# Kernel optimization log

Measured on AMD Instinct MI355X. Metric: run time of the kernel, lower is better.

## Reference

```python
import jax, jax.numpy as jnp
import numpy as np

H = 256  # hidden size

def setup_inputs() -> dict:
    key = jax.random.key(0)
    k1, k2, k3 = jax.random.split(key, 3)
    B, T, D = 64, 2048, 256
    x = jax.random.normal(k1, (B, T, D), dtype=jnp.float32)
    Wx = jax.random.normal(k2, (D, 4 * H), dtype=jnp.float32) * (1.0 / np.sqrt(D))
    Wh = jax.random.normal(k3, (H, 4 * H), dtype=jnp.float32) * (1.0 / np.sqrt(H))
    bx = jnp.zeros((4 * H,), dtype=jnp.float32)
    bh = jnp.zeros((4 * H,), dtype=jnp.float32)
    return {"x": x, "Wx": Wx, "Wh": Wh, "bx": bx, "bh": bh}

def reference(x, Wx, Wh, bx, bh):
    B, T, D = x.shape
    # Precompute input projections for all timesteps: [T, B, 4H]
    xg = jnp.einsum('btd,dg->tbg', x, Wx) + bx

    def step(carry, xg_t):
        h_prev, c_prev = carry
        gates = xg_t + h_prev @ Wh + bh          # [B, 4H]
        f, i, o, chat = jnp.split(gates, 4, axis=-1)
        f_t = jax.nn.sigmoid(f)
        i_t = jax.nn.sigmoid(i)
        o_t = jax.nn.sigmoid(o)
        c_t = f_t * c_prev + i_t * jnp.tanh(chat)
        h_t = o_t * jnp.tanh(c_t)
        return (h_t, c_t), h_t

    h0 = jnp.zeros((B, H), dtype=x.dtype)
    c0 = jnp.zeros((B, H), dtype=x.dtype)
    (h_T, c_T), hs = jax.lax.scan(step, (h0, c0), xg)  # hs: [T, B, H]
    outputs = jnp.transpose(hs, (1, 0, 2))  # batch_first: [B, T, H]
    return outputs, (h_T, c_T)
```

## Files before the change

kernel.cpp:

```cpp
#include <hip/hip_runtime.h>
#include <stdint.h>

#define H 256
#define BB 64
#define TT 2048
#define G4 1024
#define LDX 264

typedef __attribute__((ext_vector_type(8))) short short8;
typedef __attribute__((ext_vector_type(4))) float float4_;
typedef unsigned long long ull;
typedef unsigned short ushort_t;
typedef unsigned int uint_t;

static __device__ __forceinline__ float bfhi2f(ushort_t u) {
    union { unsigned int i; float f; } v; v.i = ((unsigned int)u) << 16; return v.f;
}
static __device__ __forceinline__ ushort_t f2bf(float x) {
    union { float f; unsigned int i; } v; v.f = x;
    unsigned int u = v.i;
    return (ushort_t)((u + 0x7FFFu + ((u >> 16) & 1u)) >> 16);
}
static __device__ __forceinline__ void split2(float x, ushort_t& hi, ushort_t& lo) {
    hi = f2bf(x);
    lo = f2bf(x - bfhi2f(hi));
}
static __device__ __forceinline__ float sigm(float x) { return 1.0f / (1.0f + __expf(-x)); }
static __device__ __forceinline__ float tanh_(float x) { return 2.0f / (1.0f + __expf(-2.0f * x)) - 1.0f; }

__global__ __launch_bounds__(256) void split_w(const float* __restrict__ Wx,
                                               const float* __restrict__ Wh,
                                               ushort_t* __restrict__ planes) {
    const int g = blockIdx.x & 1023;
    const int mat = blockIdx.x >> 10;
    const int k = threadIdx.x;
    const float* src = mat ? Wh : Wx;
    float v = src[(size_t)k * G4 + g];
    ushort_t hi, lo; split2(v, hi, lo);
    ushort_t* ph = planes + (size_t)mat * 2 * G4 * 256;
    ph[g * 256 + k] = hi;
    ph[(size_t)G4 * 256 + g * 256 + k] = lo;
}

__global__ __launch_bounds__(256, 1) void lstm_scan(
        const float* __restrict__ x,
        const float* __restrict__ bx,
        const float* __restrict__ bh,
        const ushort_t* __restrict__ WxTh, const ushort_t* __restrict__ WxTl,
        const ushort_t* __restrict__ WhTh, const ushort_t* __restrict__ WhTl,
        float* __restrict__ out0,
        float* __restrict__ outh,
        float* __restrict__ outc,
        uint_t* __restrict__ hbuf) {
    __shared__ ushort_t xah[16 * LDX], xal[16 * LDX];
    __shared__ ushort_t hsh[16 * LDX], hsl[16 * LDX];
    __shared__ float gatesL[1024];
    __shared__ float cst[256];
    __shared__ float bL[64];

    const int tid = threadIdx.x;
    const int grp = blockIdx.x & 3;
    const int s = blockIdx.x >> 2;
    const int lane = tid & 63, wave = tid >> 6;
    const int lm = lane & 15, lq = lane >> 4;
    const int pb = tid >> 4, pj = tid & 15;

    if (tid < 64) {
        int g = ((tid >> 4) << 8) + (s << 4) + (tid & 15);
        bL[tid] = bx[g] + bh[g];
    }
    cst[tid] = 0.0f;

    const size_t wrow = ((size_t)((wave << 8) + (s << 4) + lm)) * 256;
    short8 fxh[8], fxl[8], fhh[8], fhl[8];
#pragma unroll
    for (int kc = 0; kc < 8; ++kc) {
        fxh[kc] = *(const short8*)(WxTh + wrow + kc * 32 + lq * 8);
        fxl[kc] = *(const short8*)(WxTl + wrow + kc * 32 + lq * 8);
        fhh[kc] = *(const short8*)(WhTh + wrow + kc * 32 + lq * 8);
        fhl[kc] = *(const short8*)(WhTl + wrow + kc * 32 + lq * 8);
    }

    const float* xp0 = x + ((size_t)(grp * 16 + pb)) * TT * 256 + pj * 16;
    float* o0 = out0 + ((size_t)(grp * 16 + pb)) * TT * H + (s << 4) + pj;

    float4_ xv[4];
#pragma unroll
    for (int q = 0; q < 4; ++q) xv[q] = *(const float4_*)(xp0 + q * 4);

    const int rb = pb * LDX + pj * 16;

    for (int t = 0; t < TT; ++t) {
#pragma unroll
        for (int q = 0; q < 4; ++q) {
            union { ushort_t u[4]; ull q8; } ph_, pl_;
#pragma unroll
            for (int e = 0; e < 4; ++e) {
                ushort_t hi, lo; split2(xv[q][e], hi, lo);
                ph_.u[e] = hi; pl_.u[e] = lo;
            }
            *(ull*)(xah + rb + q * 4) = ph_.q8;
            *(ull*)(xal + rb + q * 4) = pl_.q8;
        }
        __syncthreads();

        const uint_t* hp = hbuf + ((((t & 1) << 2) + grp) << 12) + (pb << 8) + (pj << 4);
        uint_t w[16];
        if (t > 0) {
#pragma unroll
            for (int e = 0; e < 16; ++e)
                w[e] = __hip_atomic_load(hp + e, __ATOMIC_RELAXED, __HIP_MEMORY_SCOPE_AGENT);
        }

        float4_ acc = {};
#pragma unroll
        for (int kc = 0; kc < 8; ++kc) {
            short8 ah = *(const short8*)(xah + lm * LDX + kc * 32 + lq * 8);
            short8 al = *(const short8*)(xal + lm * LDX + kc * 32 + lq * 8);
            acc = __builtin_amdgcn_mfma_f32_16x16x32_bf16(ah, fxh[kc], acc, 0, 0, 0);
            acc = __builtin_amdgcn_mfma_f32_16x16x32_bf16(ah, fxl[kc], acc, 0, 0, 0);
            acc = __builtin_amdgcn_mfma_f32_16x16x32_bf16(al, fxh[kc], acc, 0, 0, 0);
        }

        if (t + 1 < TT) {
            const float* xp = xp0 + (size_t)(t + 1) * 256;
#pragma unroll
            for (int q = 0; q < 4; ++q) xv[q] = *(const float4_*)(xp + q * 4);
        }

        if (t > 0) {
            const uint_t texp = (uint_t)(t & 127);
            while (true) {
                bool ok = true;
#pragma unroll
                for (int e = 0; e < 16; ++e) ok &= ((w[e] & 127u) == texp);
                if (ok) break;
#pragma unroll
                for (int e = 0; e < 16; ++e)
                    w[e] = __hip_atomic_load(hp + e, __ATOMIC_RELAXED, __HIP_MEMORY_SCOPE_AGENT);
            }
#pragma unroll
            for (int q = 0; q < 4; ++q) {
                union { ushort_t u[4]; ull q8; } ph_, pl_;
#pragma unroll
                for (int e = 0; e < 4; ++e) {
                    float v = __uint_as_float(w[q * 4 + e] & ~127u);
                    ushort_t hi, lo; split2(v, hi, lo);
                    ph_.u[e] = hi; pl_.u[e] = lo;
                }
                *(ull*)(hsh + rb + q * 4) = ph_.q8;
                *(ull*)(hsl + rb + q * 4) = pl_.q8;
            }
            __syncthreads();

#pragma unroll
            for (int kc = 0; kc < 8; ++kc) {
                short8 ah = *(const short8*)(hsh + lm * LDX + kc * 32 + lq * 8);
                short8 al = *(const short8*)(hsl + lm * LDX + kc * 32 + lq * 8);
                acc = __builtin_amdgcn_mfma_f32_16x16x32_bf16(ah, fhh[kc], acc, 0, 0, 0);
                acc = __builtin_amdgcn_mfma_f32_16x16x32_bf16(ah, fhl[kc], acc, 0, 0, 0);
                acc = __builtin_amdgcn_mfma_f32_16x16x32_bf16(al, fhh[kc], acc, 0, 0, 0);
            }
        }

#pragma unroll
        for (int r = 0; r < 4; ++r)
            gatesL[(wave << 8) + ((lq * 4 + r) << 4) + lm] = acc[r];
        __syncthreads();

        float g0 = gatesL[tid]       + bL[pj];
        float g1 = gatesL[256 + tid] + bL[16 + pj];
        float g2 = gatesL[512 + tid] + bL[32 + pj];
        float g3 = gatesL[768 + tid] + bL[48 + pj];
        float ft = sigm(g0), it = sigm(g1), ot = sigm(g2), ch = tanh_(g3);
        float c = ft * cst[tid] + it * ch;
        cst[tid] = c;
        float hv = ot * tanh_(c);

        uint_t um = __float_as_uint(hv) & ~127u;
        float hm = __uint_as_float(um);
        o0[(size_t)t * H] = hm;

        uint_t* hw = hbuf + (((((t & 1) ^ 1) << 2) + grp) << 12) + (pb << 8) + (s << 4) + pj;
        __hip_atomic_store(hw, um | (uint_t)((t + 1) & 127), __ATOMIC_RELAXED, __HIP_MEMORY_SCOPE_AGENT);

        if (t == TT - 1) {
            outh[(grp * 16 + pb) * H + (s << 4) + pj] = hm;
            outc[(grp * 16 + pb) * H + (s << 4) + pj] = c;
        }
    }
}

extern "C" void kernel_launch(void* const* d_in, const int* in_sizes, int n_in,
                              void* d_out, int out_size, void* d_ws, size_t ws_size,
                              hipStream_t stream) {
    (void)in_sizes; (void)n_in; (void)out_size; (void)ws_size;
    const float* x  = (const float*)d_in[0];
    const float* Wx = (const float*)d_in[1];
    const float* Wh = (const float*)d_in[2];
    const float* bx = (const float*)d_in[3];
    const float* bh = (const float*)d_in[4];
    float* out0 = (float*)d_out;
    float* outh = out0 + (size_t)BB * TT * H;
    float* outc = outh + (size_t)BB * H;

    uint_t* hbuf = (uint_t*)d_ws;
    ushort_t* planes = (ushort_t*)((char*)d_ws + 131072 + 128);

    hipMemsetAsync(d_ws, 0, 131072 + 128, stream);
    split_w<<<2048, 256, 0, stream>>>(Wx, Wh, planes);
    lstm_scan<<<64, 256, 0, stream>>>(x, bx, bh,
        planes,
        planes + (size_t)G4 * 256,
        planes + (size_t)2 * G4 * 256,
        planes + (size_t)3 * G4 * 256,
        out0, outh, outc, hbuf);
}
```

Measured before the change: 8.482 ms.

## Place batch groups on single XCDs via hardware IDs and poll h through local cache

The kernel now launches 256 blocks. Each block reads its hardware ID and XCC ID, and after a global rendezvous the blocks elect 64 workers so that each batch group of 16 sits on one XCD where possible, with the spares exiting. When a group fits entirely on one XCD, the per-step h exchange is written with workgroup-scope stores and polled with sc0 loads, aiming to stay in the XCD-local L2 instead of paying agent-scope coherence latency. An agent-scope mirror buffer is kept as a fallback after 1024 failed polls, and the next-x prefetch moves to after the spin wait. This depends on undocumented cache-coherence behaviour and on all 256 blocks being co-resident, so it could deadlock or read stale data.

```diff
diff --git a/kernel.cpp b/kernel.cpp
--- a/kernel.cpp
+++ b/kernel.cpp
@@ -12,6 +12,7 @@
 typedef unsigned long long ull;
 typedef unsigned short ushort_t;
 typedef unsigned int uint_t;
+typedef __attribute__((ext_vector_type(4))) uint_t uint4_;
 
 static __device__ __forceinline__ float bfhi2f(ushort_t u) {
     union { unsigned int i; float f; } v; v.i = ((unsigned int)u) << 16; return v.f;
@@ -51,16 +52,76 @@
         float* __restrict__ out0,
         float* __restrict__ outh,
         float* __restrict__ outc,
-        uint_t* __restrict__ hbuf) {
+        uint_t* __restrict__ hbuf,
+        uint_t* __restrict__ mbuf,
+        uint_t* __restrict__ ctrl) {
     __shared__ ushort_t xah[16 * LDX], xal[16 * LDX];
     __shared__ ushort_t hsh[16 * LDX], hsl[16 * LDX];
     __shared__ float gatesL[1024];
     __shared__ float cst[256];
     __shared__ float bL[64];
+    __shared__ int Lg, Ls, Lmode;
 
     const int tid = threadIdx.x;
-    const int grp = blockIdx.x & 3;
-    const int s = blockIdx.x >> 2;
+
+    uint_t* table = ctrl + 16;
+    if (tid == 0) {
+        uint_t hwid = __builtin_amdgcn_s_getreg(63492);
+        uint_t xcc  = __builtin_amdgcn_s_getreg(63508) & 7u;
+        uint_t cuKey = (hwid >> 8) & 0xFFu;
+        __hip_atomic_store(&table[blockIdx.x], 1u | (xcc << 1) | (cuKey << 4),
+                           __ATOMIC_RELAXED, __HIP_MEMORY_SCOPE_AGENT);
+        __hip_atomic_fetch_add(&ctrl[0], 1u, __ATOMIC_RELEASE, __HIP_MEMORY_SCOPE_AGENT);
+        while (__hip_atomic_load(&ctrl[0], __ATOMIC_ACQUIRE, __HIP_MEMORY_SCOPE_AGENT) < 256u)
+            __builtin_amdgcn_s_sleep(2);
+    }
+    __syncthreads();
+    uint_t* tabL = (uint_t*)gatesL;
+    tabL[tid] = __hip_atomic_load(&table[tid], __ATOMIC_RELAXED, __HIP_MEMORY_SCOPE_AGENT);
+    __syncthreads();
+
+    if (tid == 0) {
+        int myg = -1, mys = -1, fmode = 0;
+        int cntx[8]; for (int i = 0; i < 8; ++i) cntx[i] = 0;
+        for (int b = 0; b < 256; ++b) cntx[(tabL[b] >> 1) & 7]++;
+        int host[4]; unsigned usedx = 0;
+        for (int g = 0; g < 4; ++g) {
+            int best = -1;
+            for (int xx = 0; xx < 8; ++xx)
+                if (!((usedx >> xx) & 1) && (best < 0 || cntx[xx] > cntx[best])) best = xx;
+            host[g] = best; usedx |= 1u << best;
+        }
+        unsigned taken[8]; for (int i = 0; i < 8; ++i) taken[i] = 0;
+        for (int g = 0; g < 4; ++g) {
+            int mem[16]; int n = 0; unsigned keys[16]; int allhost = 1;
+            for (int b = 0; b < 256 && n < 16; ++b) {
+                if ((taken[b >> 5] >> (b & 31)) & 1) continue;
+                uint_t e = tabL[b]; if ((int)((e >> 1) & 7) != host[g]) continue;
+                unsigned ck = (e >> 4) & 0xFFu; int dup = 0;
+                for (int q = 0; q < n; ++q) if (keys[q] == ck) { dup = 1; break; }
+                if (dup) continue;
+                keys[n] = ck; mem[n++] = b; taken[b >> 5] |= 1u << (b & 31);
+            }
+            for (int b = 0; b < 256 && n < 16; ++b) {
+                if ((taken[b >> 5] >> (b & 31)) & 1) continue;
+                uint_t e = tabL[b]; if ((int)((e >> 1) & 7) != host[g]) continue;
+                mem[n++] = b; taken[b >> 5] |= 1u << (b & 31);
+            }
+            for (int b = 0; b < 256 && n < 16; ++b) {
+                if ((taken[b >> 5] >> (b & 31)) & 1) continue;
+                mem[n++] = b; taken[b >> 5] |= 1u << (b & 31); allhost = 0;
+            }
+            for (int q = 0; q < 16; ++q)
+                if (mem[q] == (int)blockIdx.x) { myg = g; mys = q; fmode = allhost; }
+        }
+        Lg = myg; Ls = mys; Lmode = fmode;
+    }
+    __syncthreads();
+    if (Lg < 0) return;
+    const int grp = Lg, s = Ls;
+    const int fastmode = Lmode;
+    __syncthreads();
+
     const int lane = tid & 63, wave = tid >> 6;
     const int lm = lane & 15, lq = lane >> 4;
     const int pb = tid >> 4, pj = tid & 15;
@@ -89,6 +150,7 @@
     for (int q = 0; q < 4; ++q) xv[q] = *(const float4_*)(xp0 + q * 4);
 
     const int rb = pb * LDX + pj * 16;
+    int fastpoll = fastmode;
 
     for (int t = 0; t < TT; ++t) {
 #pragma unroll
@@ -103,14 +165,6 @@
             *(ull*)(xal + rb + q * 4) = pl_.q8;
         }
         __syncthreads();
-
-        const uint_t* hp = hbuf + ((((t & 1) << 2) + grp) << 12) + (pb << 8) + (pj << 4);
-        uint_t w[16];
-        if (t > 0) {
-#pragma unroll
-            for (int e = 0; e < 16; ++e)
-                w[e] = __hip_atomic_load(hp + e, __ATOMIC_RELAXED, __HIP_MEMORY_SCOPE_AGENT);
-        }
 
         float4_ acc = {};
 #pragma unroll
@@ -122,22 +176,51 @@
             acc = __builtin_amdgcn_mfma_f32_16x16x32_bf16(al, fxh[kc], acc, 0, 0, 0);
         }
 
-        if (t + 1 < TT) {
-            const float* xp = xp0 + (size_t)(t + 1) * 256;
-#pragma unroll
-            for (int q = 0; q < 4; ++q) xv[q] = *(const float4_*)(xp + q * 4);
-        }
-
         if (t > 0) {
+            const size_t ridx = ((size_t)((((t & 1) << 2) + grp) << 12)) + (pb << 8) + (pj << 4);
+            const uint_t* hp = hbuf + ridx;
+            const uint_t* mp = mbuf + ridx;
             const uint_t texp = (uint_t)(t & 127);
-            while (true) {
-                bool ok = true;
-#pragma unroll
-                for (int e = 0; e < 16; ++e) ok &= ((w[e] & 127u) == texp);
-                if (ok) break;
-#pragma unroll
-                for (int e = 0; e < 16; ++e)
-                    w[e] = __hip_atomic_load(hp + e, __ATOMIC_RELAXED, __HIP_MEMORY_SCOPE_AGENT);
+            uint_t w[16];
+            int got = 0;
+            if (fastpoll) {
+                int rounds = 0;
+                while (true) {
+                    uint4_ a0, a1, a2, a3;
+                    asm volatile(
+                        "global_load_dwordx4 %0, %4, off sc0\n\t"
+                        "global_load_dwordx4 %1, %4, off offset:16 sc0\n\t"
+                        "global_load_dwordx4 %2, %4, off offset:32 sc0\n\t"
+                        "global_load_dwordx4 %3, %4, off offset:48 sc0\n\t"
+                        "s_waitcnt vmcnt(0)"
+                        : "=&v"(a0), "=&v"(a1), "=&v"(a2), "=&v"(a3)
+                        : "v"(hp) : "memory");
+                    bool ok = true;
+#pragma unroll
+                    for (int e = 0; e < 4; ++e) {
+                        ok &= ((a0[e] & 127u) == texp); ok &= ((a1[e] & 127u) == texp);
+                        ok &= ((a2[e] & 127u) == texp); ok &= ((a3[e] & 127u) == texp);
+                    }
+                    if (ok) {
+#pragma unroll
+                        for (int e = 0; e < 4; ++e) {
+                            w[e] = a0[e]; w[4 + e] = a1[e]; w[8 + e] = a2[e]; w[12 + e] = a3[e];
+                        }
+                        got = 1; break;
+                    }
+                    if (++rounds > 1024) { fastpoll = 0; break; }
+                }
+            }
+            if (!got) {
+                while (true) {
+                    bool ok = true;
+#pragma unroll
+                    for (int e = 0; e < 16; ++e)
+                        w[e] = __hip_atomic_load(mp + e, __ATOMIC_RELAXED, __HIP_MEMORY_SCOPE_AGENT);
+#pragma unroll
+                    for (int e = 0; e < 16; ++e) ok &= ((w[e] & 127u) == texp);
+                    if (ok) break;
+                }
             }
 #pragma unroll
             for (int q = 0; q < 4; ++q) {
@@ -153,6 +236,12 @@
             }
             __syncthreads();
 
+            if (t + 1 < TT) {
+                const float* xp = xp0 + (size_t)(t + 1) * 256;
+#pragma unroll
+                for (int q = 0; q < 4; ++q) xv[q] = *(const float4_*)(xp + q * 4);
+            }
+
 #pragma unroll
             for (int kc = 0; kc < 8; ++kc) {
                 short8 ah = *(const short8*)(hsh + lm * LDX + kc * 32 + lq * 8);
@@ -161,6 +250,10 @@
                 acc = __builtin_amdgcn_mfma_f32_16x16x32_bf16(ah, fhl[kc], acc, 0, 0, 0);
                 acc = __builtin_amdgcn_mfma_f32_16x16x32_bf16(al, fhh[kc], acc, 0, 0, 0);
             }
+        } else {
+            const float* xp = xp0 + (size_t)256;
+#pragma unroll
+            for (int q = 0; q < 4; ++q) xv[q] = *(const float4_*)(xp + q * 4);
         }
 
 #pragma unroll
@@ -181,8 +274,11 @@
         float hm = __uint_as_float(um);
         o0[(size_t)t * H] = hm;
 
-        uint_t* hw = hbuf + (((((t & 1) ^ 1) << 2) + grp) << 12) + (pb << 8) + (s << 4) + pj;
-        __hip_atomic_store(hw, um | (uint_t)((t + 1) & 127), __ATOMIC_RELAXED, __HIP_MEMORY_SCOPE_AGENT);
+        const uint_t tagged = um | (uint_t)((t + 1) & 127);
+        const size_t widx = ((size_t)(((((t & 1) ^ 1) << 2) + grp) << 12)) + (pb << 8) + (s << 4) + pj;
+        if (fastmode)
+            __hip_atomic_store(hbuf + widx, tagged, __ATOMIC_RELAXED, __HIP_MEMORY_SCOPE_WORKGROUP);
+        __hip_atomic_store(mbuf + widx, tagged, __ATOMIC_RELAXED, __HIP_MEMORY_SCOPE_AGENT);
 
         if (t == TT - 1) {
             outh[(grp * 16 + pb) * H + (s << 4) + pj] = hm;
@@ -205,14 +301,16 @@
     float* outc = outh + (size_t)BB * H;
 
     uint_t* hbuf = (uint_t*)d_ws;
-    ushort_t* planes = (ushort_t*)((char*)d_ws + 131072 + 128);
-
-    hipMemsetAsync(d_ws, 0, 131072 + 128, stream);
+    uint_t* mbuf = (uint_t*)((char*)d_ws + 131072);
+    uint_t* ctrl = (uint_t*)((char*)d_ws + 262144);
+    ushort_t* planes = (ushort_t*)((char*)d_ws + 264192);
+
+    hipMemsetAsync(d_ws, 0, 264192, stream);
     split_w<<<2048, 256, 0, stream>>>(Wx, Wh, planes);
-    lstm_scan<<<64, 256, 0, stream>>>(x, bx, bh,
+    lstm_scan<<<256, 256, 0, stream>>>(x, bx, bh,
         planes,
         planes + (size_t)G4 * 256,
         planes + (size_t)2 * G4 * 256,
         planes + (size_t)3 * G4 * 256,
-        out0, outh, outc, hbuf);
-}
+        out0, outh, outc, hbuf, mbuf, ctrl);
+}
```

Result: slower. 14.95 ms (+76.3%).
